# Optimization experiments

Measured on AMD Instinct MI355X. Metric: run time of the kernel, lower is better.

The kernel has to match this reference:

```python
import jax, jax.numpy as jnp
import numpy as np


def causal_conv1d(x, w, b, dilation):
    # x: [B, Cin, S], w: [Cout, Cin, K] -> [B, Cout, S]
    # left pad by dilation*(K-1): equivalent to pad-both-sides + Chomp1d
    pad = dilation * (w.shape[-1] - 1)
    out = jax.lax.conv_general_dilated(
        x, w, window_strides=(1,), padding=[(pad, 0)],
        rhs_dilation=(dilation,), dimension_numbers=('NCH', 'OIH', 'NCH'))
    return out + b[None, :, None]


def temporal_block(x, w1, b1, w2, b2, dilation, ds=None):
    # dropout is identity in eval mode
    out = jax.nn.elu(causal_conv1d(x, w1, b1, dilation))
    out = jax.nn.elu(causal_conv1d(out, w2, b2, dilation))
    if ds is None:
        res = x
    else:
        ds_w, ds_b = ds
        res = causal_conv1d(x, ds_w, ds_b, 1)  # 1x1 downsample conv
    return jax.nn.elu(out + res)


def setup_inputs() -> dict:
    key = jax.random.key(0)
    ks = jax.random.split(key, 12)
    B, Cin, S, C, K, L = 16, 64, 4096, 128, 2, 5
    return {
        'x': jax.random.normal(ks[0], (B, Cin, S), jnp.float32),
        'w1_0': jax.random.normal(ks[1], (C, Cin, K), jnp.float32),
        'b1_0': jax.random.normal(ks[2], (C,), jnp.float32),
        'w2_0': jax.random.normal(ks[3], (C, C, K), jnp.float32),
        'b2_0': jax.random.normal(ks[4], (C,), jnp.float32),
        'ds_w': jax.random.normal(ks[5], (C, Cin, 1), jnp.float32),
        'ds_b': jax.random.normal(ks[6], (C,), jnp.float32),
        'W1': jax.random.normal(ks[7], (L - 1, C, C, K), jnp.float32),
        'B1': jax.random.normal(ks[8], (L - 1, C), jnp.float32),
        'W2': jax.random.normal(ks[9], (L - 1, C, C, K), jnp.float32),
        'B2': jax.random.normal(ks[10], (L - 1, C), jnp.float32),
    }


def reference(x, w1_0, b1_0, w2_0, b2_0, ds_w, ds_b, W1, B1, W2, B2):
    STEP = 3
    num_levels = 1 + W1.shape[0]  # 5
    outputs = [x]
    # layer 0: dilation 1, with downsample (64 -> 128 channels)
    x = temporal_block(x, w1_0, b1_0, w2_0, b2_0, 1, ds=(ds_w, ds_b))
    outputs.append(x)
    # layers 1..L-1: dilation 2**i, no downsample (128 -> 128)
    for i in range(1, num_levels):
        x = temporal_block(x, W1[i - 1], B1[i - 1], W2[i - 1], B2[i - 1], 2 ** i)
        outputs.append(x)
        if i >= STEP and outputs[i - STEP].shape == x.shape:
            x = x + outputs[i - STEP]
    return x
```

## Files before the change

### kernel.cpp

```cpp
#include <hip/hip_runtime.h>
#include <hip/hip_bf16.h>
#include <math.h>


typedef __attribute__((ext_vector_type(8))) short short8;
typedef __attribute__((ext_vector_type(4))) short short4v;
typedef __attribute__((ext_vector_type(4))) float floatx4;

#define S_LEN 4096
#define ACT_STRIDE 128
#define ROWS 192
#define AREG (ROWS * ACT_STRIDE)
#define WBUF (128 * 128)
#define LDS_BYTES ((2 * AREG + 2 * WBUF) * 2)

#define SW(row, col) ((col) ^ (((row) & 7) << 3))

#define OFF_DS     0
#define OFF_L0C1_0 8192
#define OFF_L0C1_1 16384
#define OFF_L0C2_0 24576
#define OFF_L0C2_1 40960
#define OFF_C1B    57344
#define OFF_C2B    188416

__device__ __forceinline__ float elu_f(float v) {
    return v > 0.0f ? v : (__expf(v) - 1.0f);
}
__device__ __forceinline__ short f2bs(float v) {
    __hip_bfloat16 h = __float2bfloat16(v);
    return *reinterpret_cast<short*>(&h);
}
__device__ __forceinline__ float bs2f(short s) {
    __hip_bfloat16 h = *reinterpret_cast<__hip_bfloat16*>(&s);
    return __bfloat162float(h);
}
__device__ __forceinline__ short4v pack4(const floatx4 v) {
    __hip_bfloat162 p0 = __float22bfloat162_rn(make_float2(v[0], v[1]));
    __hip_bfloat162 p1 = __float22bfloat162_rn(make_float2(v[2], v[3]));
    short4v r;
    r[0] = ((const short*)&p0)[0]; r[1] = ((const short*)&p0)[1];
    r[2] = ((const short*)&p1)[0]; r[3] = ((const short*)&p1)[1];
    return r;
}

__device__ __forceinline__ void gld_lds16(const void* g, void* l) {
    __builtin_amdgcn_global_load_lds(
        (const __attribute__((address_space(1))) void*)g,
        (__attribute__((address_space(3))) void*)l, 16, 0, 0);
}

template<int NSH>
__device__ __forceinline__ void stage_async(short* __restrict__ lds,
                                            const short* __restrict__ src,
                                            int wave, int lane)
{
    constexpr int NI = (NSH * 2) / 16384;
    const char* g = (const char*)src + wave * 1024 + lane * 16;
    char* l = (char*)lds + wave * 1024;
    #pragma unroll
    for (int i = 0; i < NI; ++i)
        gld_lds16(g + i * 16384, l + i * 16384);
}

template<int KCH>
__device__ __forceinline__ void conv_tap(
    const short* __restrict__ Lin, const short* __restrict__ Lw,
    const int doff, const int srow, const int l16, const int quad,
    const int cobase, floatx4 (&acc)[2][3])
{
    #pragma unroll
    for (int kc = 0; kc < KCH; ++kc) {
        const int col  = kc * 32 + quad * 8;
        const int wcol = SW(l16, col);
        short8 wf[2];
        #pragma unroll
        for (int mt = 0; mt < 2; ++mt)
            wf[mt] = *(const short8*)(Lw + (cobase + mt * 16 + l16) * (KCH * 32) + wcol);
        #pragma unroll
        for (int nt = 0; nt < 3; ++nt) {
            int r = srow + nt * 16 + l16 - doff;
            if (r < 0) r = 0;
            const short8 bf = *(const short8*)(Lin + r * ACT_STRIDE + SW(r, col));
            #pragma unroll
            for (int mt = 0; mt < 2; ++mt)
                acc[mt][nt] = __builtin_amdgcn_mfma_f32_16x16x32_bf16(wf[mt], bf, acc[mt][nt], 0, 0, 0);
        }
    }
}

__device__ __forceinline__ void zero_acc(floatx4 (&acc)[2][3]) {
    #pragma unroll
    for (int mt = 0; mt < 2; ++mt)
        #pragma unroll
        for (int nt = 0; nt < 3; ++nt) acc[mt][nt] = {0.f, 0.f, 0.f, 0.f};
}

template<int MODE, bool KEEP>
__device__ __forceinline__ void store_tile(short* __restrict__ dst,
    const floatx4 (&acc)[2][3], const float* __restrict__ bias,
    int cobase, int srow, int l16, int quad, int zero_below, short4v* keep)
{
    #pragma unroll
    for (int mt = 0; mt < 2; ++mt) {
        const int co4 = cobase + mt * 16 + quad * 4;
        const floatx4 bb = *(const floatx4*)(bias + co4);
        #pragma unroll
        for (int nt = 0; nt < 3; ++nt) {
            const int sl = srow + nt * 16 + l16;
            short* p = dst + sl * ACT_STRIDE + SW(sl, co4);
            floatx4 y;
            #pragma unroll
            for (int rr = 0; rr < 4; ++rr) {
                float v = acc[mt][nt][rr] + bb[rr];
                if (MODE != 1) v = elu_f(v);
                y[rr] = v;
            }
            if (MODE == 2) {
                const short4v old = *(const short4v*)p;
                #pragma unroll
                for (int rr = 0; rr < 4; ++rr) y[rr] = elu_f(y[rr] + bs2f(old[rr]));
            }
            if (sl < zero_below) y = {0.f, 0.f, 0.f, 0.f};
            const short4v pk = pack4(y);
            *(short4v*)p = pk;
            if (KEEP) keep[mt * 3 + nt] = pk;
        }
    }
}

__global__ __launch_bounds__(1024, 4)
void tcn_fused(const float* __restrict__ x,
               const short* __restrict__ wq,
               const float* __restrict__ b1_0, const float* __restrict__ b2_0,
               const float* __restrict__ ds_b, const float* __restrict__ B1,
               const float* __restrict__ B2, float* __restrict__ out)
{
    extern __shared__ short L[];
    short* RA = L;
    short* RB = L + AREG;
    short* W0 = L + 2 * AREG;
    short* W1 = L + 2 * AREG + WBUF;

    const int tid  = threadIdx.x;
    const int wave = tid >> 6, lane = tid & 63;
    const int l16  = lane & 15, quad = lane >> 4;
    const int cobase = (wave & 3) * 32;
    const int srow   = (wave >> 2) * 48;
    const int s0  = blockIdx.x * 128;
    const int s0g = s0 - 64;
    const int b   = blockIdx.y;
    const int zb  = (s0 == 0) ? 64 : 0;

    stage_async<8192>(W0, wq + OFF_DS, wave, lane);
    {
        const float* xp = x + (size_t)b * 64 * S_LEN;
        #pragma unroll
        for (int h = 0; h < 3; ++h) {
            const int r = lane + h * 64;
            const int s = s0g + r;
            short4v pk;
            #pragma unroll
            for (int c4 = 0; c4 < 4; ++c4) {
                const float v = (s >= 0) ? xp[(wave * 4 + c4) * S_LEN + s] : 0.f;
                pk[c4] = f2bs(v);
            }
            *(short4v*)(RA + r * ACT_STRIDE + SW(r, wave * 4)) = pk;
        }
    }

    floatx4 acc[2][3];
    short4v x1keep[6];

    __syncthreads();
    stage_async<8192>(W1, wq + OFF_L0C1_0, wave, lane);
    zero_acc(acc);
    conv_tap<2>(RA, W0, 0, srow, l16, quad, cobase, acc);
    store_tile<1, false>(RB, acc, ds_b, cobase, srow, l16, quad, zb, nullptr);

    __syncthreads();
    stage_async<8192>(W0, wq + OFF_L0C1_1, wave, lane);
    zero_acc(acc);
    conv_tap<2>(RA, W1, 1, srow, l16, quad, cobase, acc);

    __syncthreads();
    stage_async<16384>(W1, wq + OFF_L0C2_0, wave, lane);
    conv_tap<2>(RA, W0, 0, srow, l16, quad, cobase, acc);
    __syncthreads();
    store_tile<0, false>(RA, acc, b1_0, cobase, srow, l16, quad, zb, nullptr);

    __syncthreads();
    stage_async<16384>(W0, wq + OFF_L0C2_1, wave, lane);
    zero_acc(acc);
    conv_tap<4>(RA, W1, 1, srow, l16, quad, cobase, acc);

    __syncthreads();
    stage_async<16384>(W1, wq + OFF_C1B, wave, lane);
    conv_tap<4>(RA, W0, 0, srow, l16, quad, cobase, acc);
    store_tile<2, true>(RB, acc, b2_0, cobase, srow, l16, quad, zb, x1keep);

    #pragma unroll
    for (int lvl = 0; lvl < 3; ++lvl) {
        const int d = 2 << lvl;
        const short* nc1k1 = wq + OFF_C1B + lvl * 32768 + 16384;
        const short* nc2k0 = wq + OFF_C2B + lvl * 32768;
        const short* nc2k1 = nc2k0 + 16384;
        const short* nnext = wq + OFF_C1B + (lvl + 1) * 32768;
        __syncthreads();
        stage_async<16384>(W0, nc1k1, wave, lane);
        zero_acc(acc);
        conv_tap<4>(RB, W1, d, srow, l16, quad, cobase, acc);
        __syncthreads();
        stage_async<16384>(W1, nc2k0, wave, lane);
        conv_tap<4>(RB, W0, 0, srow, l16, quad, cobase, acc);
        store_tile<0, false>(RA, acc, B1 + lvl * 128, cobase, srow, l16, quad, zb, nullptr);
        __syncthreads();
        stage_async<16384>(W0, nc2k1, wave, lane);
        zero_acc(acc);
        conv_tap<4>(RA, W1, d, srow, l16, quad, cobase, acc);
        __syncthreads();
        stage_async<16384>(W1, nnext, wave, lane);
        conv_tap<4>(RA, W0, 0, srow, l16, quad, cobase, acc);
        store_tile<2, false>(RB, acc, B2 + lvl * 128, cobase, srow, l16, quad, zb, nullptr);
    }

    __syncthreads();
    stage_async<16384>(W0, wq + OFF_C1B + 3 * 32768 + 16384, wave, lane);
    zero_acc(acc);
    conv_tap<4>(RB, W1, 16, srow, l16, quad, cobase, acc);
    __syncthreads();
    stage_async<16384>(W1, wq + OFF_C2B + 3 * 32768, wave, lane);
    conv_tap<4>(RB, W0, 0, srow, l16, quad, cobase, acc);
    store_tile<0, false>(RA, acc, B1 + 384, cobase, srow, l16, quad, zb, nullptr);
    __syncthreads();
    stage_async<16384>(W0, wq + OFF_C2B + 3 * 32768 + 16384, wave, lane);
    zero_acc(acc);
    conv_tap<4>(RA, W1, 16, srow, l16, quad, cobase, acc);
    __syncthreads();
    conv_tap<4>(RA, W0, 0, srow, l16, quad, cobase, acc);
    {
        #pragma unroll
        for (int mt = 0; mt < 2; ++mt) {
            const int co4 = cobase + mt * 16 + quad * 4;
            const floatx4 bb = *(const floatx4*)(B2 + 384 + co4);
            #pragma unroll
            for (int nt = 0; nt < 3; ++nt) {
                if (srow + nt * 16 < 64) continue;
                const int sl = srow + nt * 16 + l16;
                const int sg = s0g + sl;
                const short4v res = *(const short4v*)(RB + sl * ACT_STRIDE + SW(sl, co4));
                const short4v k   = x1keep[mt * 3 + nt];
                #pragma unroll
                for (int rr = 0; rr < 4; ++rr) {
                    float y = elu_f(acc[mt][nt][rr] + bb[rr]);
                    y = elu_f(y + bs2f(res[rr]));
                    y += bs2f(k[rr]);
                    out[((size_t)(b * 128 + co4 + rr)) * S_LEN + sg] = y;
                }
            }
        }
    }
}

__global__ __launch_bounds__(256)
void prep_w(const float* __restrict__ w1_0, const float* __restrict__ w2_0,
            const float* __restrict__ ds_w, const float* __restrict__ W1,
            const float* __restrict__ W2, short* __restrict__ wq)
{
    int idx = blockIdx.x * 256 + threadIdx.x;
    const int n_c1 = 128 * 64;
    const int n_c2 = 128 * 128;
    if (idx < n_c1) {
        const int co = idx >> 6, ci = idx & 63;
        const int d = co * 64 + (ci ^ ((co & 7) << 3));
        wq[OFF_L0C1_0 + d] = f2bs(w1_0[idx * 2]);
        wq[OFF_L0C1_1 + d] = f2bs(w1_0[idx * 2 + 1]);
        return;
    }
    idx -= n_c1;
    if (idx < n_c2) {
        const int co = idx >> 7, ci = idx & 127;
        const int d = co * 128 + (ci ^ ((co & 7) << 3));
        wq[OFF_L0C2_0 + d] = f2bs(w2_0[idx * 2]);
        wq[OFF_L0C2_1 + d] = f2bs(w2_0[idx * 2 + 1]);
        return;
    }
    idx -= n_c2;
    if (idx < 4 * n_c2) {
        const int li = idx / n_c2, j = idx - li * n_c2;
        const int co = j >> 7, ci = j & 127;
        const int d = co * 128 + (ci ^ ((co & 7) << 3));
        wq[OFF_C1B + li * 32768 + d]         = f2bs(W1[(li * n_c2 + j) * 2]);
        wq[OFF_C1B + li * 32768 + 16384 + d] = f2bs(W1[(li * n_c2 + j) * 2 + 1]);
        return;
    }
    idx -= 4 * n_c2;
    if (idx < 4 * n_c2) {
        const int li = idx / n_c2, j = idx - li * n_c2;
        const int co = j >> 7, ci = j & 127;
        const int d = co * 128 + (ci ^ ((co & 7) << 3));
        wq[OFF_C2B + li * 32768 + d]         = f2bs(W2[(li * n_c2 + j) * 2]);
        wq[OFF_C2B + li * 32768 + 16384 + d] = f2bs(W2[(li * n_c2 + j) * 2 + 1]);
        return;
    }
    idx -= 4 * n_c2;
    if (idx < n_c1) {
        const int co = idx >> 6, ci = idx & 63;
        const int d = co * 64 + (ci ^ ((co & 7) << 3));
        wq[OFF_DS + d] = f2bs(ds_w[idx]);
    }
}

extern "C" void kernel_launch(void* const* d_in, const int* in_sizes, int n_in,
                              void* d_out, int out_size, void* d_ws, size_t ws_size,
                              hipStream_t stream) {
    const float* x_in = (const float*)d_in[0];
    const float* w1_0 = (const float*)d_in[1];
    const float* b1_0 = (const float*)d_in[2];
    const float* w2_0 = (const float*)d_in[3];
    const float* b2_0 = (const float*)d_in[4];
    const float* ds_w = (const float*)d_in[5];
    const float* ds_b = (const float*)d_in[6];
    const float* W1   = (const float*)d_in[7];
    const float* B1   = (const float*)d_in[8];
    const float* W2   = (const float*)d_in[9];
    const float* B2   = (const float*)d_in[10];
    float* out = (float*)d_out;

    short* wq = (short*)d_ws;

    (void)hipFuncSetAttribute((const void*)tcn_fused,
                              hipFuncAttributeMaxDynamicSharedMemorySize, LDS_BYTES);

    prep_w<<<dim3(640), 256, 0, stream>>>(w1_0, w2_0, ds_w, W1, W2, wq);
    tcn_fused<<<dim3(32, 16), dim3(1024), LDS_BYTES, stream>>>(
        x_in, wq, b1_0, b2_0, ds_b, B1, B2, out);
}
```

Before: 183.4 us.

## Load conv weights from global into registers instead of staging through LDS

Weight fragments are now read straight from global memory into per-wave register arrays (double-buffered wA/wB), replacing the async global-to-LDS staging buffers. This removes the barriers that guarded weight-buffer reuse and frees LDS, which now holds an extra region for the layer-0 output used in the final residual instead of keeping it in registers. Weights are stored unswizzled in the prep kernel. The cost is more VGPRs for the weight fragments at a 1024-thread block size, and weight loads that now depend on L2 latency.

```diff
diff --git a/kernel.cpp b/kernel.cpp
--- a/kernel.cpp
+++ b/kernel.cpp
@@ -11,8 +11,7 @@
 #define ACT_STRIDE 128
 #define ROWS 192
 #define AREG (ROWS * ACT_STRIDE)
-#define WBUF (128 * 128)
-#define LDS_BYTES ((2 * AREG + 2 * WBUF) * 2)
+#define LDS_BYTES (3 * AREG * 2)
 
 #define SW(row, col) ((col) ^ (((row) & 7) << 3))
 
@@ -44,39 +43,28 @@
     return r;
 }
 
-__device__ __forceinline__ void gld_lds16(const void* g, void* l) {
-    __builtin_amdgcn_global_load_lds(
-        (const __attribute__((address_space(1))) void*)g,
-        (__attribute__((address_space(3))) void*)l, 16, 0, 0);
-}
-
-template<int NSH>
-__device__ __forceinline__ void stage_async(short* __restrict__ lds,
-                                            const short* __restrict__ src,
-                                            int wave, int lane)
-{
-    constexpr int NI = (NSH * 2) / 16384;
-    const char* g = (const char*)src + wave * 1024 + lane * 16;
-    char* l = (char*)lds + wave * 1024;
-    #pragma unroll
-    for (int i = 0; i < NI; ++i)
-        gld_lds16(g + i * 16384, l + i * 16384);
+template<int KCH>
+__device__ __forceinline__ void load_w(short8 (&w)[2][4],
+                                       const short* __restrict__ wt,
+                                       int cobase, int l16, int quad)
+{
+    const short* base = wt + (cobase + l16) * (KCH * 32) + quad * 8;
+    #pragma unroll
+    for (int mt = 0; mt < 2; ++mt)
+        #pragma unroll
+        for (int kc = 0; kc < KCH; ++kc)
+            w[mt][kc] = *(const short8*)(base + mt * 16 * KCH * 32 + kc * 32);
 }
 
 template<int KCH>
 __device__ __forceinline__ void conv_tap(
-    const short* __restrict__ Lin, const short* __restrict__ Lw,
+    const short* __restrict__ Lin, const short8 (&w)[2][4],
     const int doff, const int srow, const int l16, const int quad,
-    const int cobase, floatx4 (&acc)[2][3])
+    floatx4 (&acc)[2][3])
 {
     #pragma unroll
     for (int kc = 0; kc < KCH; ++kc) {
-        const int col  = kc * 32 + quad * 8;
-        const int wcol = SW(l16, col);
-        short8 wf[2];
-        #pragma unroll
-        for (int mt = 0; mt < 2; ++mt)
-            wf[mt] = *(const short8*)(Lw + (cobase + mt * 16 + l16) * (KCH * 32) + wcol);
+        const int col = kc * 32 + quad * 8;
         #pragma unroll
         for (int nt = 0; nt < 3; ++nt) {
             int r = srow + nt * 16 + l16 - doff;
@@ -84,7 +72,7 @@
             const short8 bf = *(const short8*)(Lin + r * ACT_STRIDE + SW(r, col));
             #pragma unroll
             for (int mt = 0; mt < 2; ++mt)
-                acc[mt][nt] = __builtin_amdgcn_mfma_f32_16x16x32_bf16(wf[mt], bf, acc[mt][nt], 0, 0, 0);
+                acc[mt][nt] = __builtin_amdgcn_mfma_f32_16x16x32_bf16(w[mt][kc], bf, acc[mt][nt], 0, 0, 0);
         }
     }
 }
@@ -99,7 +87,8 @@
 template<int MODE, bool KEEP>
 __device__ __forceinline__ void store_tile(short* __restrict__ dst,
     const floatx4 (&acc)[2][3], const float* __restrict__ bias,
-    int cobase, int srow, int l16, int quad, int zero_below, short4v* keep)
+    int cobase, int srow, int l16, int quad, int zero_below,
+    short* __restrict__ x1dst)
 {
     #pragma unroll
     for (int mt = 0; mt < 2; ++mt) {
@@ -108,7 +97,8 @@
         #pragma unroll
         for (int nt = 0; nt < 3; ++nt) {
             const int sl = srow + nt * 16 + l16;
-            short* p = dst + sl * ACT_STRIDE + SW(sl, co4);
+            const int off = sl * ACT_STRIDE + SW(sl, co4);
+            short* p = dst + off;
             floatx4 y;
             #pragma unroll
             for (int rr = 0; rr < 4; ++rr) {
@@ -124,7 +114,7 @@
             if (sl < zero_below) y = {0.f, 0.f, 0.f, 0.f};
             const short4v pk = pack4(y);
             *(short4v*)p = pk;
-            if (KEEP) keep[mt * 3 + nt] = pk;
+            if (KEEP) *(short4v*)(x1dst + off) = pk;
         }
     }
 }
@@ -139,8 +129,7 @@
     extern __shared__ short L[];
     short* RA = L;
     short* RB = L + AREG;
-    short* W0 = L + 2 * AREG;
-    short* W1 = L + 2 * AREG + WBUF;
+    short* X1 = L + 2 * AREG;
 
     const int tid  = threadIdx.x;
     const int wave = tid >> 6, lane = tid & 63;
@@ -152,7 +141,10 @@
     const int b   = blockIdx.y;
     const int zb  = (s0 == 0) ? 64 : 0;
 
-    stage_async<8192>(W0, wq + OFF_DS, wave, lane);
+    short8 wA[2][4], wB[2][4];
+    floatx4 acc[2][3];
+
+    load_w<2>(wA, wq + OFF_DS, cobase, l16, quad);
     {
         const float* xp = x + (size_t)b * 64 * S_LEN;
         #pragma unroll
@@ -168,76 +160,60 @@
             *(short4v*)(RA + r * ACT_STRIDE + SW(r, wave * 4)) = pk;
         }
     }
-
-    floatx4 acc[2][3];
-    short4v x1keep[6];
-
-    __syncthreads();
-    stage_async<8192>(W1, wq + OFF_L0C1_0, wave, lane);
-    zero_acc(acc);
-    conv_tap<2>(RA, W0, 0, srow, l16, quad, cobase, acc);
+    __syncthreads();
+
+    load_w<2>(wB, wq + OFF_L0C1_0, cobase, l16, quad);
+    zero_acc(acc);
+    conv_tap<2>(RA, wA, 0, srow, l16, quad, acc);
     store_tile<1, false>(RB, acc, ds_b, cobase, srow, l16, quad, zb, nullptr);
 
-    __syncthreads();
-    stage_async<8192>(W0, wq + OFF_L0C1_1, wave, lane);
-    zero_acc(acc);
-    conv_tap<2>(RA, W1, 1, srow, l16, quad, cobase, acc);
-
-    __syncthreads();
-    stage_async<16384>(W1, wq + OFF_L0C2_0, wave, lane);
-    conv_tap<2>(RA, W0, 0, srow, l16, quad, cobase, acc);
+    load_w<2>(wA, wq + OFF_L0C1_1, cobase, l16, quad);
+    zero_acc(acc);
+    conv_tap<2>(RA, wB, 1, srow, l16, quad, acc);
+    load_w<4>(wB, wq + OFF_L0C2_0, cobase, l16, quad);
+    conv_tap<2>(RA, wA, 0, srow, l16, quad, acc);
     __syncthreads();
     store_tile<0, false>(RA, acc, b1_0, cobase, srow, l16, quad, zb, nullptr);
-
-    __syncthreads();
-    stage_async<16384>(W0, wq + OFF_L0C2_1, wave, lane);
-    zero_acc(acc);
-    conv_tap<4>(RA, W1, 1, srow, l16, quad, cobase, acc);
-
-    __syncthreads();
-    stage_async<16384>(W1, wq + OFF_C1B, wave, lane);
-    conv_tap<4>(RA, W0, 0, srow, l16, quad, cobase, acc);
-    store_tile<2, true>(RB, acc, b2_0, cobase, srow, l16, quad, zb, x1keep);
+    __syncthreads();
+
+    load_w<4>(wA, wq + OFF_L0C2_1, cobase, l16, quad);
+    zero_acc(acc);
+    conv_tap<4>(RA, wB, 1, srow, l16, quad, acc);
+    load_w<4>(wB, wq + OFF_C1B, cobase, l16, quad);
+    conv_tap<4>(RA, wA, 0, srow, l16, quad, acc);
+    store_tile<2, true>(RB, acc, b2_0, cobase, srow, l16, quad, zb, X1);
+    __syncthreads();
 
     #pragma unroll
     for (int lvl = 0; lvl < 3; ++lvl) {
         const int d = 2 << lvl;
-        const short* nc1k1 = wq + OFF_C1B + lvl * 32768 + 16384;
-        const short* nc2k0 = wq + OFF_C2B + lvl * 32768;
-        const short* nc2k1 = nc2k0 + 16384;
-        const short* nnext = wq + OFF_C1B + (lvl + 1) * 32768;
-        __syncthreads();
-        stage_async<16384>(W0, nc1k1, wave, lane);
+        load_w<4>(wA, wq + OFF_C1B + lvl * 32768 + 16384, cobase, l16, quad);
         zero_acc(acc);
-        conv_tap<4>(RB, W1, d, srow, l16, quad, cobase, acc);
-        __syncthreads();
-        stage_async<16384>(W1, nc2k0, wave, lane);
-        conv_tap<4>(RB, W0, 0, srow, l16, quad, cobase, acc);
+        conv_tap<4>(RB, wB, d, srow, l16, quad, acc);
+        load_w<4>(wB, wq + OFF_C2B + lvl * 32768, cobase, l16, quad);
+        conv_tap<4>(RB, wA, 0, srow, l16, quad, acc);
         store_tile<0, false>(RA, acc, B1 + lvl * 128, cobase, srow, l16, quad, zb, nullptr);
         __syncthreads();
-        stage_async<16384>(W0, nc2k1, wave, lane);
+        load_w<4>(wA, wq + OFF_C2B + lvl * 32768 + 16384, cobase, l16, quad);
         zero_acc(acc);
-        conv_tap<4>(RA, W1, d, srow, l16, quad, cobase, acc);
+        conv_tap<4>(RA, wB, d, srow, l16, quad, acc);
+        load_w<4>(wB, wq + OFF_C1B + (lvl + 1) * 32768, cobase, l16, quad);
+        conv_tap<4>(RA, wA, 0, srow, l16, quad, acc);
+        store_tile<2, false>(RB, acc, B2 + lvl * 128, cobase, srow, l16, quad, zb, nullptr);
         __syncthreads();
-        stage_async<16384>(W1, nnext, wave, lane);
-        conv_tap<4>(RA, W0, 0, srow, l16, quad, cobase, acc);
-        store_tile<2, false>(RB, acc, B2 + lvl * 128, cobase, srow, l16, quad, zb, nullptr);
-    }
-
-    __syncthreads();
-    stage_async<16384>(W0, wq + OFF_C1B + 3 * 32768 + 16384, wave, lane);
-    zero_acc(acc);
-    conv_tap<4>(RB, W1, 16, srow, l16, quad, cobase, acc);
-    __syncthreads();
-    stage_async<16384>(W1, wq + OFF_C2B + 3 * 32768, wave, lane);
-    conv_tap<4>(RB, W0, 0, srow, l16, quad, cobase, acc);
+    }
+
+    load_w<4>(wA, wq + OFF_C1B + 3 * 32768 + 16384, cobase, l16, quad);
+    zero_acc(acc);
+    conv_tap<4>(RB, wB, 16, srow, l16, quad, acc);
+    load_w<4>(wB, wq + OFF_C2B + 3 * 32768, cobase, l16, quad);
+    conv_tap<4>(RB, wA, 0, srow, l16, quad, acc);
     store_tile<0, false>(RA, acc, B1 + 384, cobase, srow, l16, quad, zb, nullptr);
     __syncthreads();
-    stage_async<16384>(W0, wq + OFF_C2B + 3 * 32768 + 16384, wave, lane);
-    zero_acc(acc);
-    conv_tap<4>(RA, W1, 16, srow, l16, quad, cobase, acc);
-    __syncthreads();
-    conv_tap<4>(RA, W0, 0, srow, l16, quad, cobase, acc);
+    load_w<4>(wA, wq + OFF_C2B + 3 * 32768 + 16384, cobase, l16, quad);
+    zero_acc(acc);
+    conv_tap<4>(RA, wB, 16, srow, l16, quad, acc);
+    conv_tap<4>(RA, wA, 0, srow, l16, quad, acc);
     {
         #pragma unroll
         for (int mt = 0; mt < 2; ++mt) {
@@ -248,8 +224,9 @@
                 if (srow + nt * 16 < 64) continue;
                 const int sl = srow + nt * 16 + l16;
                 const int sg = s0g + sl;
-                const short4v res = *(const short4v*)(RB + sl * ACT_STRIDE + SW(sl, co4));
-                const short4v k   = x1keep[mt * 3 + nt];
+                const int off = sl * ACT_STRIDE + SW(sl, co4);
+                const short4v res = *(const short4v*)(RB + off);
+                const short4v k   = *(const short4v*)(X1 + off);
                 #pragma unroll
                 for (int rr = 0; rr < 4; ++rr) {
                     float y = elu_f(acc[mt][nt][rr] + bb[rr]);
@@ -271,44 +248,32 @@
     const int n_c1 = 128 * 64;
     const int n_c2 = 128 * 128;
     if (idx < n_c1) {
-        const int co = idx >> 6, ci = idx & 63;
-        const int d = co * 64 + (ci ^ ((co & 7) << 3));
-        wq[OFF_L0C1_0 + d] = f2bs(w1_0[idx * 2]);
-        wq[OFF_L0C1_1 + d] = f2bs(w1_0[idx * 2 + 1]);
+        wq[OFF_L0C1_0 + idx] = f2bs(w1_0[idx * 2]);
+        wq[OFF_L0C1_1 + idx] = f2bs(w1_0[idx * 2 + 1]);
         return;
     }
     idx -= n_c1;
     if (idx < n_c2) {
-        const int co = idx >> 7, ci = idx & 127;
-        const int d = co * 128 + (ci ^ ((co & 7) << 3));
-        wq[OFF_L0C2_0 + d] = f2bs(w2_0[idx * 2]);
-        wq[OFF_L0C2_1 + d] = f2bs(w2_0[idx * 2 + 1]);
+        wq[OFF_L0C2_0 + idx] = f2bs(w2_0[idx * 2]);
+        wq[OFF_L0C2_1 + idx] = f2bs(w2_0[idx * 2 + 1]);
         return;
     }
     idx -= n_c2;
     if (idx < 4 * n_c2) {
         const int li = idx / n_c2, j = idx - li * n_c2;
-        const int co = j >> 7, ci = j & 127;
-        const int d = co * 128 + (ci ^ ((co & 7) << 3));
-        wq[OFF_C1B + li * 32768 + d]         = f2bs(W1[(li * n_c2 + j) * 2]);
-        wq[OFF_C1B + li * 32768 + 16384 + d] = f2bs(W1[(li * n_c2 + j) * 2 + 1]);
+        wq[OFF_C1B + li * 32768 + j]         = f2bs(W1[(li * n_c2 + j) * 2]);
+        wq[OFF_C1B + li * 32768 + 16384 + j] = f2bs(W1[(li * n_c2 + j) * 2 + 1]);
         return;
     }
     idx -= 4 * n_c2;
     if (idx < 4 * n_c2) {
         const int li = idx / n_c2, j = idx - li * n_c2;
-        const int co = j >> 7, ci = j & 127;
-        const int d = co * 128 + (ci ^ ((co & 7) << 3));
-        wq[OFF_C2B + li * 32768 + d]         = f2bs(W2[(li * n_c2 + j) * 2]);
-        wq[OFF_C2B + li * 32768 + 16384 + d] = f2bs(W2[(li * n_c2 + j) * 2 + 1]);
+        wq[OFF_C2B + li * 32768 + j]         = f2bs(W2[(li * n_c2 + j) * 2]);
+        wq[OFF_C2B + li * 32768 + 16384 + j] = f2bs(W2[(li * n_c2 + j) * 2 + 1]);
         return;
     }
     idx -= 4 * n_c2;
-    if (idx < n_c1) {
-        const int co = idx >> 6, ci = idx & 63;
-        const int d = co * 64 + (ci ^ ((co & 7) << 3));
-        wq[OFF_DS + d] = f2bs(ds_w[idx]);
-    }
+    if (idx < n_c1) wq[OFF_DS + idx] = f2bs(ds_w[idx]);
 }
 
 extern "C" void kernel_launch(void* const* d_in, const int* in_sizes, int n_in,
```

After: 246.4 us. 1.34x slower.

## Store activations and weights in MFMA fragment-blocked LDS layout

Applied to the files above, without the earlier changes.

Replaces the XOR-swizzled row-major LDS layout for activations and weights with a layout blocked to match the 16x16x32 MFMA fragments. Each lane's 8-element operand now sits in a contiguous, linearly addressed slot, which removes the per-load swizzle arithmetic. All weight fragments for a tap are also hoisted into registers before looping over N tiles. The goal is fewer address calculations and conflict-free LDS reads, at the cost of more VGPRs and changed store patterns that may cause bank conflicts in the epilogue writes.

```diff
diff --git a/kernel.cpp b/kernel.cpp
--- a/kernel.cpp
+++ b/kernel.cpp
@@ -8,13 +8,10 @@
 typedef __attribute__((ext_vector_type(4))) float floatx4;
 
 #define S_LEN 4096
-#define ACT_STRIDE 128
 #define ROWS 192
-#define AREG (ROWS * ACT_STRIDE)
+#define AREG (ROWS * 128)
 #define WBUF (128 * 128)
 #define LDS_BYTES ((2 * AREG + 2 * WBUF) * 2)
-
-#define SW(row, col) ((col) ^ (((row) & 7) << 3))
 
 #define OFF_DS     0
 #define OFF_L0C1_0 8192
@@ -69,22 +66,25 @@
     const int doff, const int srow, const int l16, const int quad,
     const int cobase, floatx4 (&acc)[2][3])
 {
-    #pragma unroll
-    for (int kc = 0; kc < KCH; ++kc) {
-        const int col  = kc * 32 + quad * 8;
-        const int wcol = SW(l16, col);
-        short8 wf[2];
-        #pragma unroll
-        for (int mt = 0; mt < 2; ++mt)
-            wf[mt] = *(const short8*)(Lw + (cobase + mt * 16 + l16) * (KCH * 32) + wcol);
-        #pragma unroll
-        for (int nt = 0; nt < 3; ++nt) {
-            int r = srow + nt * 16 + l16 - doff;
-            if (r < 0) r = 0;
-            const short8 bf = *(const short8*)(Lin + r * ACT_STRIDE + SW(r, col));
+    const short* wb = Lw + (cobase >> 4) * (KCH * 512) + quad * 128 + l16 * 8;
+    short8 wf[2][4];
+    #pragma unroll
+    for (int mt = 0; mt < 2; ++mt)
+        #pragma unroll
+        for (int kc = 0; kc < KCH; ++kc)
+            wf[mt][kc] = *(const short8*)(wb + mt * (KCH * 512) + kc * 512);
+
+    #pragma unroll
+    for (int nt = 0; nt < 3; ++nt) {
+        int r = srow + nt * 16 + l16 - doff;
+        if (r < 0) r = 0;
+        const short* ab = Lin + (r >> 4) * 2048 + (r & 15) * 8 + quad * 128;
+        #pragma unroll
+        for (int kc = 0; kc < KCH; ++kc) {
+            const short8 bf = *(const short8*)(ab + kc * 512);
             #pragma unroll
             for (int mt = 0; mt < 2; ++mt)
-                acc[mt][nt] = __builtin_amdgcn_mfma_f32_16x16x32_bf16(wf[mt], bf, acc[mt][nt], 0, 0, 0);
+                acc[mt][nt] = __builtin_amdgcn_mfma_f32_16x16x32_bf16(wf[mt][kc], bf, acc[mt][nt], 0, 0, 0);
         }
     }
 }
@@ -104,11 +104,12 @@
     #pragma unroll
     for (int mt = 0; mt < 2; ++mt) {
         const int co4 = cobase + mt * 16 + quad * 4;
+        const int cterm = (co4 >> 5) * 512 + ((co4 >> 3) & 3) * 128 + (co4 & 7);
         const floatx4 bb = *(const floatx4*)(bias + co4);
         #pragma unroll
         for (int nt = 0; nt < 3; ++nt) {
             const int sl = srow + nt * 16 + l16;
-            short* p = dst + sl * ACT_STRIDE + SW(sl, co4);
+            short* p = dst + (sl >> 4) * 2048 + (sl & 15) * 8 + cterm;
             floatx4 y;
             #pragma unroll
             for (int rr = 0; rr < 4; ++rr) {
@@ -155,6 +156,8 @@
     stage_async<8192>(W0, wq + OFF_DS, wave, lane);
     {
         const float* xp = x + (size_t)b * 64 * S_LEN;
+        const int ci0 = wave * 4;
+        const int cterm = (ci0 >> 5) * 512 + ((ci0 >> 3) & 3) * 128 + (ci0 & 7);
         #pragma unroll
         for (int h = 0; h < 3; ++h) {
             const int r = lane + h * 64;
@@ -162,10 +165,10 @@
             short4v pk;
             #pragma unroll
             for (int c4 = 0; c4 < 4; ++c4) {
-                const float v = (s >= 0) ? xp[(wave * 4 + c4) * S_LEN + s] : 0.f;
+                const float v = (s >= 0) ? xp[(ci0 + c4) * S_LEN + s] : 0.f;
                 pk[c4] = f2bs(v);
             }
-            *(short4v*)(RA + r * ACT_STRIDE + SW(r, wave * 4)) = pk;
+            *(short4v*)(RA + (r >> 4) * 2048 + (r & 15) * 8 + cterm) = pk;
         }
     }
 
@@ -242,13 +245,15 @@
         #pragma unroll
         for (int mt = 0; mt < 2; ++mt) {
             const int co4 = cobase + mt * 16 + quad * 4;
+            const int cterm = (co4 >> 5) * 512 + ((co4 >> 3) & 3) * 128 + (co4 & 7);
             const floatx4 bb = *(const floatx4*)(B2 + 384 + co4);
             #pragma unroll
             for (int nt = 0; nt < 3; ++nt) {
                 if (srow + nt * 16 < 64) continue;
                 const int sl = srow + nt * 16 + l16;
                 const int sg = s0g + sl;
-                const short4v res = *(const short4v*)(RB + sl * ACT_STRIDE + SW(sl, co4));
+                const int off = (sl >> 4) * 2048 + (sl & 15) * 8 + cterm;
+                const short4v res = *(const short4v*)(RB + off);
                 const short4v k   = x1keep[mt * 3 + nt];
                 #pragma unroll
                 for (int rr = 0; rr < 4; ++rr) {
@@ -262,6 +267,11 @@
     }
 }
 
+__device__ __forceinline__ int widx(int co, int ci, int KC) {
+    return (co >> 4) * (KC * 512) + (ci >> 5) * 512 + ((ci >> 3) & 3) * 128
+         + (co & 15) * 8 + (ci & 7);
+}
+
 __global__ __launch_bounds__(256)
 void prep_w(const float* __restrict__ w1_0, const float* __restrict__ w2_0,
             const float* __restrict__ ds_w, const float* __restrict__ W1,
@@ -272,7 +282,7 @@
     const int n_c2 = 128 * 128;
     if (idx < n_c1) {
         const int co = idx >> 6, ci = idx & 63;
-        const int d = co * 64 + (ci ^ ((co & 7) << 3));
+        const int d = widx(co, ci, 2);
         wq[OFF_L0C1_0 + d] = f2bs(w1_0[idx * 2]);
         wq[OFF_L0C1_1 + d] = f2bs(w1_0[idx * 2 + 1]);
         return;
@@ -280,7 +290,7 @@
     idx -= n_c1;
     if (idx < n_c2) {
         const int co = idx >> 7, ci = idx & 127;
-        const int d = co * 128 + (ci ^ ((co & 7) << 3));
+        const int d = widx(co, ci, 4);
         wq[OFF_L0C2_0 + d] = f2bs(w2_0[idx * 2]);
         wq[OFF_L0C2_1 + d] = f2bs(w2_0[idx * 2 + 1]);
         return;
@@ -289,7 +299,7 @@
     if (idx < 4 * n_c2) {
         const int li = idx / n_c2, j = idx - li * n_c2;
         const int co = j >> 7, ci = j & 127;
-        const int d = co * 128 + (ci ^ ((co & 7) << 3));
+        const int d = widx(co, ci, 4);
         wq[OFF_C1B + li * 32768 + d]         = f2bs(W1[(li * n_c2 + j) * 2]);
         wq[OFF_C1B + li * 32768 + 16384 + d] = f2bs(W1[(li * n_c2 + j) * 2 + 1]);
         return;
@@ -298,7 +308,7 @@
     if (idx < 4 * n_c2) {
         const int li = idx / n_c2, j = idx - li * n_c2;
         const int co = j >> 7, ci = j & 127;
-        const int d = co * 128 + (ci ^ ((co & 7) << 3));
+        const int d = widx(co, ci, 4);
         wq[OFF_C2B + li * 32768 + d]         = f2bs(W2[(li * n_c2 + j) * 2]);
         wq[OFF_C2B + li * 32768 + 16384 + d] = f2bs(W2[(li * n_c2 + j) * 2 + 1]);
         return;
@@ -306,8 +316,7 @@
     idx -= 4 * n_c2;
     if (idx < n_c1) {
         const int co = idx >> 6, ci = idx & 63;
-        const int d = co * 64 + (ci ^ ((co & 7) << 3));
-        wq[OFF_DS + d] = f2bs(ds_w[idx]);
+        wq[OFF_DS + widx(co, ci, 2)] = f2bs(ds_w[idx]);
     }
 }
 
```

New measurement: 176.3 us. 1.04x faster.
